# Kernel optimization log

Hardware: AMD Instinct MI355X
Metric: run time of the kernel (lower is better)

Reference implementation:

```python
import jax, jax.numpy as jnp
import numpy as np

V = 32000   # vocab_size
E = 512     # embedding_size
H = 512     # hidden_size
B = 32      # batch
T = 48      # caption seq_len
BOS = 1     # bos token id


def _xavier(key, shape):
    fan_out, fan_in = shape
    lim = np.sqrt(6.0 / (fan_in + fan_out)).astype(np.float32)
    return jax.random.uniform(key, shape, jnp.float32, -lim, lim)


def setup_inputs() -> dict:
    key = jax.random.key(0)
    ks = jax.random.split(key, 6)
    return {
        "image_features": jax.random.normal(ks[0], (1, B, E), jnp.float32),
        "ground_truth_captions": jax.random.randint(ks[1], (B, T), 0, V),
        "embedding": _xavier(ks[2], (V, E)),
        "W_ih": _xavier(ks[3], (4 * H, E)),
        "W_hh": _xavier(ks[4], (4 * H, H)),
        "b_ih": jnp.zeros((4 * H,), jnp.float32),
        "b_hh": jnp.zeros((4 * H,), jnp.float32),
        "W_head": _xavier(ks[5], (V, H)),
        "b_head": jnp.zeros((V,), jnp.float32),
    }


def _lstm_step(carry, x, W_ih, W_hh, b):
    # PyTorch LSTM cell: gate order i, f, g, o
    h, c = carry
    gates = x @ W_ih.T + h @ W_hh.T + b          # [B, 4H]
    i, f, g, o = jnp.split(gates, 4, axis=-1)
    c = jax.nn.sigmoid(f) * c + jax.nn.sigmoid(i) * jnp.tanh(g)
    h = jax.nn.sigmoid(o) * jnp.tanh(c)
    return (h, c), h


def reference(image_features, ground_truth_captions, embedding,
              W_ih, W_hh, b_ih, b_hh, W_head, b_head):
    b = b_ih + b_hh
    bsz = image_features.shape[1]
    step = lambda carry, x: _lstm_step(carry, x, W_ih, W_hh, b)

    # _init_step: run LSTM over image features from zero state
    h0 = jnp.zeros((bsz, H), image_features.dtype)
    c0 = jnp.zeros((bsz, H), image_features.dtype)
    (h, c), _ = jax.lax.scan(step, (h0, c0), image_features)

    # teacher-forced input tokens for steps t = 1 .. T-1:
    # [bos, gt[:,1], ..., gt[:,T-2]]  -> shape [T-1, B]
    tokens = jnp.concatenate(
        [jnp.full((1, bsz), BOS, ground_truth_captions.dtype),
         ground_truth_captions[:, 1:T - 1].T], axis=0)
    emb = embedding[tokens]                      # [T-1, B, E]

    (_, _), hs = jax.lax.scan(step, (h, c), emb)  # [T-1, B, H]
    logits = jnp.einsum('tbh,vh->tbv', hs, W_head) + b_head  # [T-1, B, V]

    # outputs[0] stays zero, as in the torch loop
    outputs = jnp.concatenate(
        [jnp.zeros((1, bsz, V), logits.dtype), logits], axis=0)
    return outputs
```

## Files before the change

kernel.cpp:

```cpp
#include <hip/hip_runtime.h>
#include <hip/hip_bf16.h>

#define V_ 32000
#define E_ 512
#define H_ 512
#define B_ 32
#define T_ 48
#define NWG 16
#define NCON 125
#define GRID (NWG + 1 + NCON)
#define SPIN_CAP (1 << 20)

typedef __attribute__((ext_vector_type(8))) short bf16x8;
typedef __attribute__((ext_vector_type(4))) float f32x4;
typedef __attribute__((ext_vector_type(4))) int   i32x4;
typedef __attribute__((ext_vector_type(2))) int   i32x2;

static __device__ __forceinline__ short f2bf(float f) {
  union { __hip_bfloat16 h; short s; } u;
  u.h = __float2bfloat16(f);
  return u.s;
}

static __device__ __forceinline__ bf16x8 load_cvt8(const float* p) {
  float4 a = *(const float4*)p;
  float4 b = *(const float4*)(p + 4);
  bf16x8 r;
  r[0] = f2bf(a.x); r[1] = f2bf(a.y); r[2] = f2bf(a.z); r[3] = f2bf(a.w);
  r[4] = f2bf(b.x); r[5] = f2bf(b.y); r[6] = f2bf(b.z); r[7] = f2bf(b.w);
  return r;
}

static __device__ __forceinline__ float sigf(float x) {
  return 1.0f / (1.0f + __expf(-x));
}
static __device__ __forceinline__ float tanh_fast(float x) {
  float e = __expf(2.0f * x);
  return (e - 1.0f) / (e + 1.0f);
}

static __device__ __forceinline__ unsigned prog_load(const unsigned* p) {
  unsigned v;
  asm volatile("global_load_dword %0, %1, off sc0 sc1\n\t"
               "s_waitcnt vmcnt(0)"
               : "=&v"(v) : "v"(p) : "memory");
  return v;
}

#define PLOADS8(T, ADDR)                                               \
  asm volatile(                                                        \
    "global_load_dwordx4 %0, %8, off sc0 sc1\n\t"                      \
    "global_load_dwordx4 %1, %8, off offset:16 sc0 sc1\n\t"            \
    "global_load_dwordx4 %2, %8, off offset:32 sc0 sc1\n\t"            \
    "global_load_dwordx4 %3, %8, off offset:48 sc0 sc1\n\t"            \
    "global_load_dwordx4 %4, %8, off offset:64 sc0 sc1\n\t"            \
    "global_load_dwordx4 %5, %8, off offset:80 sc0 sc1\n\t"            \
    "global_load_dwordx4 %6, %8, off offset:96 sc0 sc1\n\t"            \
    "global_load_dwordx4 %7, %8, off offset:112 sc0 sc1\n\t"           \
    "s_waitcnt vmcnt(0)"                                               \
    : "=&v"(T[0]), "=&v"(T[1]), "=&v"(T[2]), "=&v"(T[3]),              \
      "=&v"(T[4]), "=&v"(T[5]), "=&v"(T[6]), "=&v"(T[7])               \
    : "v"(ADDR) : "memory")

#define CLOADS4(T, ADDR)                                               \
  asm volatile(                                                        \
    "global_load_dwordx4 %0, %4, off sc0 sc1\n\t"                      \
    "global_load_dwordx4 %1, %4, off offset:16 sc0 sc1\n\t"            \
    "global_load_dwordx4 %2, %4, off offset:32 sc0 sc1\n\t"            \
    "global_load_dwordx4 %3, %4, off offset:48 sc0 sc1\n\t"            \
    "s_waitcnt vmcnt(0)"                                               \
    : "=&v"(T[0]), "=&v"(T[1]), "=&v"(T[2]), "=&v"(T[3])               \
    : "v"(ADDR) : "memory")

#define DSTORE(ADDR, VAL)                                              \
  asm volatile("global_store_dword %0, %1, off sc0 sc1"                \
               :: "v"(ADDR), "v"(VAL) : "memory")
#define DSTORE2(ADDR, VAL)                                             \
  asm volatile("global_store_dwordx2 %0, %1, off sc0 sc1"              \
               :: "v"(ADDR), "v"(VAL) : "memory")

__global__ __launch_bounds__(256) void k_xg(
    const float* __restrict__ img,
    const int*   __restrict__ gt,
    const float* __restrict__ emb,
    const float* __restrict__ W_ih,
    const float* __restrict__ b_ih,
    const float* __restrict__ b_hh,
    float* __restrict__ Xg)
{
  const int s    = blockIdx.x;
  const int lane = threadIdx.x & 63;
  const int wv   = threadIdx.x >> 6;
  const int nbase = blockIdx.y * 256 + wv * 64;
  const int lr  = lane & 15;
  const int lkb = lane >> 4;

  const float* arow[2];
#pragma unroll
  for (int m = 0; m < 2; ++m) {
    int b = m * 16 + lr;
    const float* src;
    if (s == 0) {
      src = img + b * E_;
    } else {
      int tok = (s == 1) ? 1 : gt[b * T_ + (s - 1)];
      src = emb + (long)tok * E_;
    }
    arow[m] = src;
  }

  f32x4 acc[2][4];
#pragma unroll
  for (int m = 0; m < 2; ++m)
#pragma unroll
    for (int n = 0; n < 4; ++n) acc[m][n] = (f32x4){0.f, 0.f, 0.f, 0.f};

  for (int kt = 0; kt < 16; ++kt) {
    int ko = kt * 32 + lkb * 8;
    bf16x8 a0 = load_cvt8(arow[0] + ko);
    bf16x8 a1 = load_cvt8(arow[1] + ko);
#pragma unroll
    for (int n = 0; n < 4; ++n) {
      const float* wp = W_ih + (long)(nbase + n * 16 + lr) * E_ + ko;
      bf16x8 bw = load_cvt8(wp);
      acc[0][n] = __builtin_amdgcn_mfma_f32_16x16x32_bf16(a0, bw, acc[0][n], 0, 0, 0);
      acc[1][n] = __builtin_amdgcn_mfma_f32_16x16x32_bf16(a1, bw, acc[1][n], 0, 0, 0);
    }
  }

#pragma unroll
  for (int n = 0; n < 4; ++n) {
    int j = nbase + n * 16 + lr;
    float bias = b_ih[j] + b_hh[j];
#pragma unroll
    for (int m = 0; m < 2; ++m) {
#pragma unroll
      for (int r = 0; r < 4; ++r) {
        int b = m * 16 + lkb * 4 + r;
        Xg[((long)(s * B_ + b) * 2048) + j] = acc[m][n][r] + bias;
      }
    }
  }
}

__global__ __launch_bounds__(256, 1) void k_fused(
    const float* __restrict__ W_hh,
    const float* __restrict__ Xg,
    const float* __restrict__ W_head,
    const float* __restrict__ b_head,
    unsigned* __restrict__ flags,
    unsigned* __restrict__ replicas,
    unsigned short* __restrict__ hbuf,
    unsigned short* __restrict__ hs,
    float* __restrict__ out)
{
  __shared__ __align__(16) char lds[147456];
  const int tid  = threadIdx.x;
  const int lane = tid & 63;
  const int wv   = tid >> 6;
  const int lr   = lane & 15;
  const int lkb  = lane >> 4;

  if (blockIdx.x < NWG) {
    char* wlds  = lds;
    char* stage = lds + 98304;
    char* gbufc = lds + 131072;
    const int w = blockIdx.x;
    const int g = wv;

    bf16x8 awr[2][4];
#pragma unroll
    for (int rt = 0; rt < 2; ++rt) {
      int row = g * 512 + w * 32 + rt * 16 + lr;
#pragma unroll
      for (int kt = 0; kt < 12; ++kt) {
        bf16x8 wf = load_cvt8(W_hh + (long)row * E_ + kt * 32 + lkb * 8);
        *(bf16x8*)(wlds + ((((wv * 2 + rt) * 12 + kt) * 64) + lane) * 16) = wf;
      }
#pragma unroll
      for (int kt = 12; kt < 16; ++kt)
        awr[rt][kt - 12] = load_cvt8(W_hh + (long)row * E_ + kt * 32 + lkb * 8);
    }

    const int cb_b  = tid >> 3;
    const int cb_di = (tid & 7) * 4;
    f32x4 cst = (f32x4){0.f, 0.f, 0.f, 0.f};
    __syncthreads();

    for (int t = 0; t < T_; ++t) {
      float4 xg[2][2];
#pragma unroll
      for (int rt = 0; rt < 2; ++rt)
#pragma unroll
        for (int bt = 0; bt < 2; ++bt)
          xg[rt][bt] = *(const float4*)(Xg + ((long)t * B_ + bt * 16 + lr) * 2048 +
                                        g * 512 + w * 32 + rt * 16 + lkb * 4);

      f32x4 acc[2][2];
#pragma unroll
      for (int rt = 0; rt < 2; ++rt) {
        acc[rt][0] = (f32x4){0.f, 0.f, 0.f, 0.f};
        acc[rt][1] = (f32x4){0.f, 0.f, 0.f, 0.f};
      }

      if (t > 0) {
        if (wv == 0) {
          for (int it = 0; it < SPIN_CAP; ++it) {
            unsigned v = 0xFFFFFFFFu;
            if (lane < NWG) v = prog_load(flags + lane * 32);
            if (__ballot(v >= (unsigned)t) == ~0ULL) break;
            __builtin_amdgcn_s_sleep(1);
          }
        }
        __syncthreads();

        const char* pb = (const char*)hbuf + ((t - 1) & 1) * 32768 + tid * 128;
        i32x4 u[8];
        PLOADS8(u, pb);

        int b_own = tid >> 3, j0b = (tid & 7) * 128;
#pragma unroll
        for (int c = 0; c < 8; ++c)
          *(i32x4*)(stage + b_own * 1024 + ((j0b + c * 16) ^ ((b_own & 7) << 4))) = u[c];
        __syncthreads();

#pragma unroll
        for (int kt = 0; kt < 16; ++kt) {
          int b0r = lr, b1r = 16 + lr;
          i32x4 bv0 = *(const i32x4*)(stage + b0r * 1024 +
                                      ((kt * 64 + lkb * 16) ^ ((b0r & 7) << 4)));
          i32x4 bv1 = *(const i32x4*)(stage + b1r * 1024 +
                                      ((kt * 64 + lkb * 16) ^ ((b1r & 7) << 4)));
          bf16x8 b0 = *(bf16x8*)&bv0, b1 = *(bf16x8*)&bv1;
#pragma unroll
          for (int rt = 0; rt < 2; ++rt) {
            bf16x8 a;
            if (kt < 12) a = *(const bf16x8*)(wlds +
                             ((((wv * 2 + rt) * 12 + kt) * 64) + lane) * 16);
            else a = awr[rt][kt - 12];
            acc[rt][0] = __builtin_amdgcn_mfma_f32_16x16x32_bf16(a, b0, acc[rt][0], 0, 0, 0);
            acc[rt][1] = __builtin_amdgcn_mfma_f32_16x16x32_bf16(a, b1, acc[rt][1], 0, 0, 0);
          }
        }
      }

#pragma unroll
      for (int rt = 0; rt < 2; ++rt)
#pragma unroll
        for (int bt = 0; bt < 2; ++bt) {
          int b = bt * 16 + lr;
          f32x4 r = acc[rt][bt];
          r[0] += xg[rt][bt].x; r[1] += xg[rt][bt].y;
          r[2] += xg[rt][bt].z; r[3] += xg[rt][bt].w;
          *(f32x4*)(gbufc + (g * 32 + b) * 128 +
                    (((rt * 16 + lkb * 4) * 4) ^ ((b & 7) << 4))) = r;
        }
      __syncthreads();

      int rb = (cb_di * 4) ^ ((cb_b & 7) << 4);
      float4 gi  = *(const float4*)(gbufc + (0 * 32 + cb_b) * 128 + rb);
      float4 gf  = *(const float4*)(gbufc + (1 * 32 + cb_b) * 128 + rb);
      float4 gg_ = *(const float4*)(gbufc + (2 * 32 + cb_b) * 128 + rb);
      float4 go  = *(const float4*)(gbufc + (3 * 32 + cb_b) * 128 + rb);
      float iv[4] = {gi.x, gi.y, gi.z, gi.w};
      float fv[4] = {gf.x, gf.y, gf.z, gf.w};
      float gv[4] = {gg_.x, gg_.y, gg_.z, gg_.w};
      float ov[4] = {go.x, go.y, go.z, go.w};
      unsigned short hb[4];
#pragma unroll
      for (int r = 0; r < 4; ++r) {
        float c_ = sigf(fv[r]) * cst[r] + sigf(iv[r]) * tanh_fast(gv[r]);
        cst[r] = c_;
        hb[r] = (unsigned short)f2bf(sigf(ov[r]) * tanh_fast(c_));
      }
      i32x2 pk;
      pk[0] = (int)((unsigned)hb[0] | ((unsigned)hb[1] << 16));
      pk[1] = (int)((unsigned)hb[2] | ((unsigned)hb[3] << 16));

      if (t < T_ - 1) {
        unsigned short* hn = hbuf + (t & 1) * (B_ * H_) + cb_b * H_ + w * 32 + cb_di;
        DSTORE2(hn, pk);
      } else {
        unsigned short* hp = hs + ((long)(t - 1) * B_ + cb_b) * H_ + w * 32 + cb_di;
        DSTORE2(hp, pk);
      }
      asm volatile("s_waitcnt vmcnt(0)" ::: "memory");
      __syncthreads();
      if (tid == 0) DSTORE(flags + w * 32, (unsigned)(t + 1));

      if (t >= 1 && t < T_ - 1) {
        unsigned short* hp = hs + ((long)(t - 1) * B_ + cb_b) * H_ + w * 32 + cb_di;
        DSTORE2(hp, pk);
      }
    }
  } else if (blockIdx.x == NWG) {
    if (tid < 64) {
      for (unsigned e = 2; e <= (unsigned)T_; ++e) {
        for (int it = 0; it < SPIN_CAP; ++it) {
          unsigned f = (lane < NWG) ? prog_load(flags + lane * 32) : 0xFFFFFFFFu;
          if (__ballot(f >= e) == ~0ULL) break;
          __builtin_amdgcn_s_sleep(2);
        }
        DSTORE(replicas + lane * 32, e);
      }
    }
  } else {
    char* stage = lds;
    const int cid = blockIdx.x - NWG - 1;

    bf16x8 bw[4][16];
    float bias[4];
#pragma unroll
    for (int j = 0; j < 4; ++j) {
      int v = cid * 256 + j * 64 + wv * 16 + lr;
#pragma unroll
      for (int kt = 0; kt < 16; ++kt)
        bw[j][kt] = load_cvt8(W_head + (long)v * E_ + kt * 32 + lkb * 8);
      bias[j] = b_head[v];
    }

    for (int mt = 0; mt < 94; ++mt) {
      int step = mt / 2 + 1;
      int tagneed = (step + 2 <= T_) ? (step + 2) : T_;
      if (tid == 0) {
        const unsigned* rp = replicas + (cid & 63) * 32;
        for (int it = 0; it < SPIN_CAP; ++it) {
          if (prog_load(rp) >= (unsigned)tagneed) break;
          __builtin_amdgcn_s_sleep(32);
        }
      }
      __syncthreads();

      const char* src = (const char*)(hs + (long)mt * 16 * H_) + tid * 64;
      i32x4 st[4];
      CLOADS4(st, src);
#pragma unroll
      for (int i = 0; i < 4; ++i) {
        int c = tid * 4 + i;
        int row = c >> 6;
        int cb  = (c & 63) * 16;
        *(i32x4*)(stage + row * 1024 + (cb ^ ((row & 7) << 4))) = st[i];
      }
      __syncthreads();

      f32x4 acc[4];
#pragma unroll
      for (int j = 0; j < 4; ++j)
        acc[j] = (f32x4){bias[j], bias[j], bias[j], bias[j]};
#pragma unroll
      for (int kt = 0; kt < 16; ++kt) {
        int cb = kt * 64 + lkb * 16;
        i32x4 av = *(const i32x4*)(stage + lr * 1024 + (cb ^ ((lr & 7) << 4)));
        bf16x8 a = *(bf16x8*)&av;
#pragma unroll
        for (int j = 0; j < 4; ++j)
          acc[j] = __builtin_amdgcn_mfma_f32_16x16x32_bf16(a, bw[j][kt], acc[j], 0, 0, 0);
      }

#pragma unroll
      for (int j = 0; j < 4; ++j)
#pragma unroll
        for (int r = 0; r < 4; ++r) {
          int R = mt * 16 + lkb * 4 + r;
          out[(long)(R + 32) * V_ + cid * 256 + j * 64 + wv * 16 + lr] = acc[j][r];
        }
    }
  }
}

extern "C" void kernel_launch(void* const* d_in, const int* in_sizes, int n_in,
                              void* d_out, int out_size, void* d_ws, size_t ws_size,
                              hipStream_t stream) {
  const float* img  = (const float*)d_in[0];
  const int*   gt   = (const int*)d_in[1];
  const float* emb  = (const float*)d_in[2];
  const float* W_ih = (const float*)d_in[3];
  const float* W_hh = (const float*)d_in[4];
  const float* b_ih = (const float*)d_in[5];
  const float* b_hh = (const float*)d_in[6];
  const float* W_hd = (const float*)d_in[7];
  const float* b_hd = (const float*)d_in[8];
  float* out = (float*)d_out;

  char* ws = (char*)d_ws;
  unsigned*       flags = (unsigned*)(ws);
  unsigned*       repl  = (unsigned*)(ws + 8192);
  unsigned short* hbuf  = (unsigned short*)(ws + 16384);
  unsigned short* hs    = (unsigned short*)(ws + 16384 + 65536);
  float*          Xg    = (float*)(ws + 16384 + 65536 + 1540096);

  hipMemsetAsync(ws, 0, 16384, stream);
  hipMemsetAsync(out, 0, (size_t)B_ * V_ * sizeof(float), stream);

  dim3 g1(48, 8);
  k_xg<<<g1, 256, 0, stream>>>(img, gt, emb, W_ih, b_ih, b_hh, Xg);
  k_fused<<<GRID, 256, 0, stream>>>(W_hh, Xg, W_hd, b_hd, flags, repl, hbuf, hs, out);
}
```

Baseline: 330.7 us.

## Embed step tags in hidden-state exchange to replace flag-based barrier

The 16 recurrent workgroups stop spinning on per-workgroup flags before reading the previous hidden state. Each 4-value packet of h is now stored together with its step tag in a double-buffered exchange area, and readers poll the data itself until every tag matches. This removes the store, wait, barrier and flag-write round trip from each step's critical path. In exchange each packet doubles in size, and the flags that feed the consumer replicas are now written at a different point and with new tag values.

Result: slower. 360.0 us (+8.9%).

```diff
diff --git a/kernel.cpp b/kernel.cpp
--- a/kernel.cpp
+++ b/kernel.cpp
@@ -47,19 +47,29 @@
   return v;
 }
 
-#define PLOADS8(T, ADDR)                                               \
+#define PLOADS16(T, ADDR)                                              \
   asm volatile(                                                        \
-    "global_load_dwordx4 %0, %8, off sc0 sc1\n\t"                      \
-    "global_load_dwordx4 %1, %8, off offset:16 sc0 sc1\n\t"            \
-    "global_load_dwordx4 %2, %8, off offset:32 sc0 sc1\n\t"            \
-    "global_load_dwordx4 %3, %8, off offset:48 sc0 sc1\n\t"            \
-    "global_load_dwordx4 %4, %8, off offset:64 sc0 sc1\n\t"            \
-    "global_load_dwordx4 %5, %8, off offset:80 sc0 sc1\n\t"            \
-    "global_load_dwordx4 %6, %8, off offset:96 sc0 sc1\n\t"            \
-    "global_load_dwordx4 %7, %8, off offset:112 sc0 sc1\n\t"           \
+    "global_load_dwordx4 %0,  %16, off sc0 sc1\n\t"                    \
+    "global_load_dwordx4 %1,  %16, off offset:16 sc0 sc1\n\t"          \
+    "global_load_dwordx4 %2,  %16, off offset:32 sc0 sc1\n\t"          \
+    "global_load_dwordx4 %3,  %16, off offset:48 sc0 sc1\n\t"          \
+    "global_load_dwordx4 %4,  %16, off offset:64 sc0 sc1\n\t"          \
+    "global_load_dwordx4 %5,  %16, off offset:80 sc0 sc1\n\t"          \
+    "global_load_dwordx4 %6,  %16, off offset:96 sc0 sc1\n\t"          \
+    "global_load_dwordx4 %7,  %16, off offset:112 sc0 sc1\n\t"         \
+    "global_load_dwordx4 %8,  %16, off offset:128 sc0 sc1\n\t"         \
+    "global_load_dwordx4 %9,  %16, off offset:144 sc0 sc1\n\t"         \
+    "global_load_dwordx4 %10, %16, off offset:160 sc0 sc1\n\t"         \
+    "global_load_dwordx4 %11, %16, off offset:176 sc0 sc1\n\t"         \
+    "global_load_dwordx4 %12, %16, off offset:192 sc0 sc1\n\t"         \
+    "global_load_dwordx4 %13, %16, off offset:208 sc0 sc1\n\t"         \
+    "global_load_dwordx4 %14, %16, off offset:224 sc0 sc1\n\t"         \
+    "global_load_dwordx4 %15, %16, off offset:240 sc0 sc1\n\t"         \
     "s_waitcnt vmcnt(0)"                                               \
-    : "=&v"(T[0]), "=&v"(T[1]), "=&v"(T[2]), "=&v"(T[3]),              \
-      "=&v"(T[4]), "=&v"(T[5]), "=&v"(T[6]), "=&v"(T[7])               \
+    : "=&v"(T[0]),  "=&v"(T[1]),  "=&v"(T[2]),  "=&v"(T[3]),           \
+      "=&v"(T[4]),  "=&v"(T[5]),  "=&v"(T[6]),  "=&v"(T[7]),           \
+      "=&v"(T[8]),  "=&v"(T[9]),  "=&v"(T[10]), "=&v"(T[11]),          \
+      "=&v"(T[12]), "=&v"(T[13]), "=&v"(T[14]), "=&v"(T[15])           \
     : "v"(ADDR) : "memory")
 
 #define CLOADS4(T, ADDR)                                               \
@@ -77,6 +87,9 @@
                :: "v"(ADDR), "v"(VAL) : "memory")
 #define DSTORE2(ADDR, VAL)                                             \
   asm volatile("global_store_dwordx2 %0, %1, off sc0 sc1"              \
+               :: "v"(ADDR), "v"(VAL) : "memory")
+#define QSTORE(ADDR, VAL)                                              \
+  asm volatile("global_store_dwordx4 %0, %1, off sc0 sc1"              \
                :: "v"(ADDR), "v"(VAL) : "memory")
 
 __global__ __launch_bounds__(256) void k_xg(
@@ -150,7 +163,7 @@
     const float* __restrict__ b_head,
     unsigned* __restrict__ flags,
     unsigned* __restrict__ replicas,
-    unsigned short* __restrict__ hbuf,
+    char* __restrict__ hxc,
     unsigned short* __restrict__ hs,
     float* __restrict__ out)
 {
@@ -204,25 +217,27 @@
       }
 
       if (t > 0) {
-        if (wv == 0) {
-          for (int it = 0; it < SPIN_CAP; ++it) {
-            unsigned v = 0xFFFFFFFFu;
-            if (lane < NWG) v = prog_load(flags + lane * 32);
-            if (__ballot(v >= (unsigned)t) == ~0ULL) break;
-            __builtin_amdgcn_s_sleep(1);
-          }
+        const char* pb = hxc + (t & 1) * 65536 +
+                         ((long)(tid >> 3) * 256 + (tid & 7) * 32) * 8;
+        i32x4 u[16];
+        for (int it = 0; it < SPIN_CAP; ++it) {
+          PLOADS16(u, pb);
+          bool ok = true;
+#pragma unroll
+          for (int i = 0; i < 16; ++i)
+            ok = ok && (u[i][1] == t) && (u[i][3] == t);
+          if (ok) break;
+          __builtin_amdgcn_s_sleep(1);
+        }
+        int b_own = tid >> 3, j0b = (tid & 7) * 128;
+#pragma unroll
+        for (int c = 0; c < 8; ++c) {
+          i32x4 pc = (i32x4){u[2*c][0], u[2*c][2], u[2*c+1][0], u[2*c+1][2]};
+          *(i32x4*)(stage + b_own * 1024 + ((j0b + c * 16) ^ ((b_own & 7) << 4))) = pc;
         }
         __syncthreads();
 
-        const char* pb = (const char*)hbuf + ((t - 1) & 1) * 32768 + tid * 128;
-        i32x4 u[8];
-        PLOADS8(u, pb);
-
-        int b_own = tid >> 3, j0b = (tid & 7) * 128;
-#pragma unroll
-        for (int c = 0; c < 8; ++c)
-          *(i32x4*)(stage + b_own * 1024 + ((j0b + c * 16) ^ ((b_own & 7) << 4))) = u[c];
-        __syncthreads();
+        if (tid == 0) DSTORE(flags + w * 32, (unsigned)t);
 
 #pragma unroll
         for (int kt = 0; kt < 16; ++kt) {
@@ -273,29 +288,26 @@
         cst[r] = c_;
         hb[r] = (unsigned short)f2bf(sigf(ov[r]) * tanh_fast(c_));
       }
-      i32x2 pk;
-      pk[0] = (int)((unsigned)hb[0] | ((unsigned)hb[1] << 16));
-      pk[1] = (int)((unsigned)hb[2] | ((unsigned)hb[3] << 16));
+      int pk0 = (int)((unsigned)hb[0] | ((unsigned)hb[1] << 16));
+      int pk1 = (int)((unsigned)hb[2] | ((unsigned)hb[3] << 16));
+      long ubase = (long)cb_b * 256 + w * 16 + (cb_di >> 1);
 
       if (t < T_ - 1) {
-        unsigned short* hn = hbuf + (t & 1) * (B_ * H_) + cb_b * H_ + w * 32 + cb_di;
-        DSTORE2(hn, pk);
-      } else {
-        unsigned short* hp = hs + ((long)(t - 1) * B_ + cb_b) * H_ + w * 32 + cb_di;
-        DSTORE2(hp, pk);
-      }
-      asm volatile("s_waitcnt vmcnt(0)" ::: "memory");
-      __syncthreads();
-      if (tid == 0) DSTORE(flags + w * 32, (unsigned)(t + 1));
-
-      if (t >= 1 && t < T_ - 1) {
-        unsigned short* hp = hs + ((long)(t - 1) * B_ + cb_b) * H_ + w * 32 + cb_di;
-        DSTORE2(hp, pk);
-      }
-    }
+        i32x4 unit = (i32x4){pk0, t + 1, pk1, t + 1};
+        QSTORE(hxc + ((t + 1) & 1) * 65536 + ubase * 8, unit);
+      }
+      if (t >= 1) {
+        i32x2 pk; pk[0] = pk0; pk[1] = pk1;
+        DSTORE2(hs + ((long)(t - 1) * B_ + cb_b) * H_ + w * 32 + cb_di, pk);
+      }
+    }
+    asm volatile("s_waitcnt vmcnt(0)" ::: "memory");
+    __syncthreads();
+    if (tid == 0) DSTORE(flags + w * 32, (unsigned)(T_ + 1));
+
   } else if (blockIdx.x == NWG) {
     if (tid < 64) {
-      for (unsigned e = 2; e <= (unsigned)T_; ++e) {
+      for (unsigned e = 2; e <= (unsigned)(T_ + 1); ++e) {
         for (int it = 0; it < SPIN_CAP; ++it) {
           unsigned f = (lane < NWG) ? prog_load(flags + lane * 32) : 0xFFFFFFFFu;
           if (__ballot(f >= e) == ~0ULL) break;
@@ -320,8 +332,7 @@
     }
 
     for (int mt = 0; mt < 94; ++mt) {
-      int step = mt / 2 + 1;
-      int tagneed = (step + 2 <= T_) ? (step + 2) : T_;
+      int tagneed = mt / 2 + 2;
       if (tid == 0) {
         const unsigned* rp = replicas + (cid & 63) * 32;
         for (int it = 0; it < SPIN_CAP; ++it) {
@@ -385,14 +396,14 @@
   char* ws = (char*)d_ws;
   unsigned*       flags = (unsigned*)(ws);
   unsigned*       repl  = (unsigned*)(ws + 8192);
-  unsigned short* hbuf  = (unsigned short*)(ws + 16384);
-  unsigned short* hs    = (unsigned short*)(ws + 16384 + 65536);
-  float*          Xg    = (float*)(ws + 16384 + 65536 + 1540096);
-
-  hipMemsetAsync(ws, 0, 16384, stream);
+  char*           hxc   = ws + 16384;
+  unsigned short* hs    = (unsigned short*)(ws + 147456);
+  float*          Xg    = (float*)(ws + 1687552);
+
+  hipMemsetAsync(ws, 0, 147456, stream);
   hipMemsetAsync(out, 0, (size_t)B_ * V_ * sizeof(float), stream);
 
   dim3 g1(48, 8);
   k_xg<<<g1, 256, 0, stream>>>(img, gt, emb, W_ih, b_ih, b_hh, Xg);
-  k_fused<<<GRID, 256, 0, stream>>>(W_hh, Xg, W_hd, b_hd, flags, repl, hbuf, hs, out);
-}
+  k_fused<<<GRID, 256, 0, stream>>>(W_hh, Xg, W_hd, b_hd, flags, repl, hxc, hs, out);
+}
```
